# Kernel tuning notes

Measured on AMD Instinct MI355X. Metric: run time of the kernel, lower is better.

Reference implementation:

```python
import jax, jax.numpy as jnp
import numpy as np
from jax import lax

C = 128; G = 8; K = 3; P = K * K; GC = C // G
N, H, W = 4, 96, 96
EPS = 1e-5

def conv_bn_silu(x, w, gamma, beta, rmean, rvar, stride, pad):
    # Conv2d(bias=False) + BatchNorm2d(eval) + SiLU, NCHW
    y = lax.conv_general_dilated(x, w, (stride, stride), [(pad, pad), (pad, pad)],
                                 dimension_numbers=('NCHW', 'OIHW', 'NCHW'))
    s = gamma / jnp.sqrt(rvar + EPS)
    y = y * s[None, :, None, None] + (beta - rmean * s)[None, :, None, None]
    return y * jax.nn.sigmoid(y)

def dcnv3(x, dw_w, dw_b, ln_g, ln_b, off_w, off_b, m_w, m_b, ip_w, ip_b, op_w, op_b):
    # InternImage DCNv3, channels-last input (N,H,W,C), k=3 s=1 pad=1 dil=1 group=G, offset_scale=1
    n, h, w, c = x.shape
    xp = x @ ip_w.T + ip_b  # input_proj
    # offset/mask branch: depthwise 3x3 conv + LayerNorm + GELU on the ORIGINAL input
    dw = lax.conv_general_dilated(x, dw_w, (1, 1), [(1, 1), (1, 1)],
                                  dimension_numbers=('NHWC', 'HWIO', 'NHWC'),
                                  feature_group_count=c) + dw_b
    dw = (dw - dw.mean(-1, keepdims=True)) / jnp.sqrt(dw.var(-1, keepdims=True) + EPS) * ln_g + ln_b
    dw = jax.nn.gelu(dw)
    off = (dw @ off_w.T + off_b).reshape(n, h, w, G, P, 2)  # (..., (dx, dy))
    m = jax.nn.softmax((dw @ m_w.T + m_b).reshape(n, h, w, G, P), -1)
    pad = 1
    hp, wp = h + 2 * pad, w + 2 * pad
    xpad = jnp.pad(xp, ((0, 0), (pad, pad), (pad, pad), (0, 0))).reshape(n, hp, wp, G, GC)
    ky, kx = jnp.meshgrid(jnp.arange(-1, 2, dtype=x.dtype), jnp.arange(-1, 2, dtype=x.dtype), indexing='ij')
    # absolute sampling coords in padded image (grid_sample align_corners=False equivalent)
    py = (jnp.arange(h, dtype=x.dtype) + pad)[None, :, None, None, None] + ky.reshape(-1) + off[..., 1]
    px = (jnp.arange(w, dtype=x.dtype) + pad)[None, None, :, None, None] + kx.reshape(-1) + off[..., 0]
    yf = jnp.floor(py); xf = jnp.floor(px)
    wy = py - yf; wx = px - xf
    y0 = yf.astype(jnp.int32); x0 = xf.astype(jnp.int32)
    n_idx = jnp.arange(n)[:, None, None, None, None]
    g_idx = jnp.arange(G)[None, None, None, :, None]

    def gat(yi, xi):
        valid = ((yi >= 0) & (yi < hp) & (xi >= 0) & (xi < wp)).astype(x.dtype)
        v = xpad[n_idx, jnp.clip(yi, 0, hp - 1), jnp.clip(xi, 0, wp - 1), g_idx]  # (n,h,w,G,P,GC)
        return v * valid[..., None]

    v = (gat(y0, x0) * ((1 - wy) * (1 - wx))[..., None]
         + gat(y0, x0 + 1) * ((1 - wy) * wx)[..., None]
         + gat(y0 + 1, x0) * (wy * (1 - wx))[..., None]
         + gat(y0 + 1, x0 + 1) * (wy * wx)[..., None])
    out = jnp.einsum('nhwgpc,nhwgp->nhwgc', v, m).reshape(n, h, w, c)
    return out @ op_w.T + op_b  # output_proj

def _forward(x0, x1, x2, conv_w, conv_g, conv_b, conv_rm, conv_rv,
             conv1_w, conv1_g, conv1_b, conv1_rm, conv1_rv,
             conv2_w, conv2_g, conv2_b, conv2_rm, conv2_rv,
             dw_w, dw_b, ln_g, ln_b, off_w, off_b, m_w, m_b, ip_w, ip_b, op_w, op_b):
    n, _, h, w = x0.shape
    # x1: 256 ch > 128 -> self.conv (1x1); smaller spatial -> bilinear upsample to HW
    y1 = conv_bn_silu(x1, conv_w, conv_g, conv_b, conv_rm, conv_rv, 1, 0)
    feat_up1 = jax.image.resize(y1, (n, C, h, w), method='bilinear')
    # x2: 64 ch < 128 -> self.conv1 (1x1); larger spatial -> self.conv2 (3x3 s2) to HW
    y2 = conv_bn_silu(x2, conv1_w, conv1_g, conv1_b, conv1_rm, conv1_rv, 1, 0)
    feat_up2 = conv_bn_silu(y2, conv2_w, conv2_g, conv2_b, conv2_rm, conv2_rv, 2, 1)
    d1 = dcnv3(feat_up1.transpose(0, 2, 3, 1), dw_w, dw_b, ln_g, ln_b, off_w, off_b, m_w, m_b, ip_w, ip_b, op_w, op_b)
    d2 = dcnv3(feat_up2.transpose(0, 2, 3, 1), dw_w, dw_b, ln_g, ln_b, off_w, off_b, m_w, m_b, ip_w, ip_b, op_w, op_b)
    a1 = jax.nn.relu(d1).transpose(0, 3, 1, 2)
    a2 = jax.nn.relu(d2).transpose(0, 3, 1, 2)
    return jnp.concatenate([a1, x0, a2], axis=1)  # (N, 3C, H, W)

def setup_inputs():
    ks = jax.random.split(jax.random.key(0), 24)
    f = jnp.float32
    return {
        'x0': jax.random.normal(ks[0], (N, C, H, W), f),
        'x1': jax.random.normal(ks[1], (N, 2 * C, H // 2, W // 2), f),
        'x2': jax.random.normal(ks[2], (N, C // 2, 2 * H, 2 * W), f),
        'conv_w': jax.random.normal(ks[3], (C, 2 * C, 1, 1), f) * 0.05,
        'conv_g': jnp.ones((C,), f), 'conv_b': jnp.zeros((C,), f),
        'conv_rm': jax.random.normal(ks[4], (C,), f) * 0.1,
        'conv_rv': jax.random.uniform(ks[5], (C,), f) + 0.5,
        'conv1_w': jax.random.normal(ks[6], (C, C // 2, 1, 1), f) * 0.08,
        'conv1_g': jnp.ones((C,), f), 'conv1_b': jnp.zeros((C,), f),
        'conv1_rm': jax.random.normal(ks[7], (C,), f) * 0.1,
        'conv1_rv': jax.random.uniform(ks[8], (C,), f) + 0.5,
        'conv2_w': jax.random.normal(ks[9], (C, C, 3, 3), f) * 0.03,
        'conv2_g': jnp.ones((C,), f), 'conv2_b': jnp.zeros((C,), f),
        'conv2_rm': jax.random.normal(ks[10], (C,), f) * 0.1,
        'conv2_rv': jax.random.uniform(ks[11], (C,), f) + 0.5,
        'dw_w': jax.random.normal(ks[12], (3, 3, 1, C), f) * 0.1,
        'dw_b': jnp.zeros((C,), f),
        'ln_g': jnp.ones((C,), f), 'ln_b': jnp.zeros((C,), f),
        'off_w': jax.random.normal(ks[13], (G * P * 2, C), f) * 0.01,
        'off_b': jnp.zeros((G * P * 2,), f),
        'm_w': jax.random.normal(ks[14], (G * P, C), f) * 0.05,
        'm_b': jnp.zeros((G * P,), f),
        'ip_w': jax.random.normal(ks[15], (C, C), f) * 0.05,
        'ip_b': jnp.zeros((C,), f),
        'op_w': jax.random.normal(ks[16], (C, C), f) * 0.05,
        'op_b': jnp.zeros((C,), f),
    }

def reference(x0, x1, x2, conv_w, conv_g, conv_b, conv_rm, conv_rv,
              conv1_w, conv1_g, conv1_b, conv1_rm, conv1_rv,
              conv2_w, conv2_g, conv2_b, conv2_rm, conv2_rv,
              dw_w, dw_b, ln_g, ln_b, off_w, off_b, m_w, m_b, ip_w, ip_b, op_w, op_b):
    return _forward(x0, x1, x2, conv_w, conv_g, conv_b, conv_rm, conv_rv,
                    conv1_w, conv1_g, conv1_b, conv1_rm, conv1_rv,
                    conv2_w, conv2_g, conv2_b, conv2_rm, conv2_rv,
                    dw_w, dw_b, ln_g, ln_b, off_w, off_b, m_w, m_b, ip_w, ip_b, op_w, op_b)
```

## Files before the change

### kernel.cpp

```cpp
#include <hip/hip_runtime.h>
#include <cstdint>
#include <cstddef>

#define EPSV 1e-5f
#define NPIX 9216
#define LDA 136
#define LDK 72

typedef __bf16 bf16;
typedef _Float16 f16;
typedef __attribute__((ext_vector_type(8))) __bf16 bf16x8;
typedef __attribute__((ext_vector_type(4))) __bf16 bf16x4;
typedef __attribute__((ext_vector_type(2))) _Float16 f16x2;
typedef __attribute__((ext_vector_type(4))) float  f32x4;

__device__ __forceinline__ float silu_f(float v) { return v / (1.f + __expf(-v)); }

__global__ __launch_bounds__(256) void prep_kernel(
    const float* __restrict__ conv_w, const float* __restrict__ conv_g,
    const float* __restrict__ conv_b, const float* __restrict__ conv_rm, const float* __restrict__ conv_rv,
    const float* __restrict__ conv1_w, const float* __restrict__ conv1_g,
    const float* __restrict__ conv1_b, const float* __restrict__ conv1_rm, const float* __restrict__ conv1_rv,
    const float* __restrict__ conv2_w, const float* __restrict__ conv2_g,
    const float* __restrict__ conv2_bb, const float* __restrict__ conv2_rm, const float* __restrict__ conv2_rv,
    const float* __restrict__ ip_w, const float* __restrict__ op_w,
    const float* __restrict__ off_w, const float* __restrict__ m_w,
    const float* __restrict__ off_b, const float* __restrict__ m_b,
    float* __restrict__ WTSf, bf16* __restrict__ WTSb)
{
  int idx = blockIdx.x * 256 + threadIdx.x;
  if (idx < 608) {
    if (idx < 128) {
      int co = idx;
      float s = conv_g[co] * rsqrtf(conv_rv[co] + EPSV);
      WTSf[idx] = conv_b[co] - conv_rm[co] * s;
    } else if (idx < 256) {
      int co = idx - 128;
      float s = conv1_g[co] * rsqrtf(conv1_rv[co] + EPSV);
      WTSf[idx] = conv1_b[co] - conv1_rm[co] * s;
    } else if (idx < 384) {
      int co = idx - 256;
      float s = conv2_g[co] * rsqrtf(conv2_rv[co] + EPSV);
      WTSf[idx] = conv2_bb[co] - conv2_rm[co] * s;
    } else {
      int col = idx - 384;
      WTSf[idx] = (col < 144) ? off_b[col] : (col < 216 ? m_b[col - 144] : 0.f);
    }
  } else {
    int j = idx - 608;
    if (j < 32768) {
      int co = j >> 8, ci = j & 255;
      float s = conv_g[co] * rsqrtf(conv_rv[co] + EPSV);
      WTSb[j] = (bf16)(conv_w[co * 256 + ci] * s);
    } else if (j < 40960) {
      int r = j - 32768; int co = r >> 6, ci = r & 63;
      float s = conv1_g[co] * rsqrtf(conv1_rv[co] + EPSV);
      WTSb[j] = (bf16)(conv1_w[co * 64 + ci] * s);
    } else if (j < 188416) {
      int r = j - 40960; int kp = r >> 14; int rr = r & 16383;
      int co = rr >> 7, ci = rr & 127;
      float s = conv2_g[co] * rsqrtf(conv2_rv[co] + EPSV);
      WTSb[j] = (bf16)(conv2_w[(co * 128 + ci) * 9 + kp] * s);
    } else if (j < 204800) {
      int r = j - 188416; int co = r >> 7, ci = r & 127;
      WTSb[j] = (bf16)ip_w[co * 128 + ci];
    } else if (j < 233472) {
      int r = j - 204800; int co = r >> 7, ci = r & 127;
      float v = (co < 144) ? off_w[co * 128 + ci] : (co < 216 ? m_w[(co - 144) * 128 + ci] : 0.f);
      WTSb[j] = (bf16)v;
    } else if (j < 249856) {
      int r = j - 233472; int co = r >> 7, ci = r & 127;
      WTSb[j] = (bf16)op_w[co * 128 + ci];
    }
  }
}

__device__ __forceinline__ void c1x1_body(
    bf16* As, bf16* Bs, const float* __restrict__ x, const bf16* __restrict__ W,
    const float* __restrict__ bias, int K, int HW, int m0, bf16* __restrict__ outb)
{
  int t = threadIdx.x;
  int n = m0 / HW; int hw0 = m0 - n * HW;
  const float* xn = x + (size_t)n * K * HW;
  int wv = t >> 6, lane = t & 63;
  int lrow = lane & 15, q = lane >> 4;
  int n0 = wv * 32;
  f32x4 acc[4][2];
#pragma unroll
  for (int i = 0; i < 4; ++i)
#pragma unroll
    for (int j = 0; j < 2; ++j)
#pragma unroll
      for (int e = 0; e < 4; ++e) acc[i][j][e] = 0.f;

  for (int k0 = 0; k0 < K; k0 += 64) {
    if (k0) __syncthreads();
    for (int i = t; i < 1024; i += 256) {
      int px = i & 63; int ci4 = (i >> 6) << 2;
      bf16x4 p;
#pragma unroll
      for (int j = 0; j < 4; ++j)
        p[j] = (bf16)xn[(size_t)(k0 + ci4 + j) * HW + hw0 + px];
      *(bf16x4*)&As[px * LDK + ci4] = p;
    }
    for (int i = t; i < 1024; i += 256) {
      int co = i >> 3; int k8 = (i & 7) << 3;
      *(bf16x8*)&Bs[co * LDK + k8] = *(const bf16x8*)&W[(size_t)co * K + k0 + k8];
    }
    __syncthreads();
#pragma unroll
    for (int ks = 0; ks < 2; ++ks) {
      int ko = ks * 32 + q * 8;
      bf16x8 bfr0 = *(const bf16x8*)&Bs[(n0 + lrow) * LDK + ko];
      bf16x8 bfr1 = *(const bf16x8*)&Bs[(n0 + 16 + lrow) * LDK + ko];
#pragma unroll
      for (int mi = 0; mi < 4; ++mi) {
        bf16x8 afr = *(const bf16x8*)&As[(mi * 16 + lrow) * LDK + ko];
        acc[mi][0] = __builtin_amdgcn_mfma_f32_16x16x32_bf16(afr, bfr0, acc[mi][0], 0, 0, 0);
        acc[mi][1] = __builtin_amdgcn_mfma_f32_16x16x32_bf16(afr, bfr1, acc[mi][1], 0, 0, 0);
      }
    }
  }
#pragma unroll
  for (int mi = 0; mi < 4; ++mi) {
#pragma unroll
    for (int nj = 0; nj < 2; ++nj) {
      int co = n0 + nj * 16 + lrow;
      float bb = bias[co];
#pragma unroll
      for (int r = 0; r < 4; ++r) {
        int m = m0 + mi * 16 + q * 4 + r;
        outb[(size_t)m * 128 + co] = (bf16)silu_f(acc[mi][nj][r] + bb);
      }
    }
  }
}

__global__ __launch_bounds__(256) void c1x1_dual_kernel(
    const float* __restrict__ x1, const bf16* __restrict__ W1b, const float* __restrict__ b1f,
    const float* __restrict__ x2, const bf16* __restrict__ W1bb, const float* __restrict__ b1bf,
    bf16* __restrict__ y1b, bf16* __restrict__ y2b)
{
  __shared__ bf16 As[64 * LDK];
  __shared__ bf16 Bs[128 * LDK];
  int bid = blockIdx.x;
  if (bid < 2304) {
    c1x1_body(As, Bs, x2, W1bb, b1bf, 64, 36864, bid << 6, y2b);
  } else {
    c1x1_body(As, Bs, x1, W1b, b1f, 256, 2304, (bid - 2304) << 6, y1b);
  }
}

__global__ __launch_bounds__(256) void upsample_kernel(
    const bf16* __restrict__ y1b, bf16* __restrict__ feat1b)
{
  int idx = blockIdx.x * 256 + threadIdx.x;
  int c4 = (idx & 31) << 2;
  int pw = idx >> 5;
  int ow = pw % 96; int t1 = pw / 96;
  int oh = t1 % 96; int n = t1 / 96;
  float sh = oh * 0.5f - 0.25f, sw = ow * 0.5f - 0.25f;
  float hf = floorf(sh), wf = floorf(sw);
  float fy = sh - hf, fx = sw - wf;
  int h0 = (int)hf, w0 = (int)wf;
  int h0c = max(h0, 0), h1c = min(h0 + 1, 47);
  int w0c = max(w0, 0), w1c = min(w0 + 1, 47);
  const bf16* yn = y1b + (size_t)n * 2304 * 128 + c4;
  bf16x4 v00 = *(const bf16x4*)&yn[(h0c * 48 + w0c) * 128];
  bf16x4 v01 = *(const bf16x4*)&yn[(h0c * 48 + w1c) * 128];
  bf16x4 v10 = *(const bf16x4*)&yn[(h1c * 48 + w0c) * 128];
  bf16x4 v11 = *(const bf16x4*)&yn[(h1c * 48 + w1c) * 128];
  bf16x4 o;
#pragma unroll
  for (int e = 0; e < 4; ++e) {
    float v = (1.f - fy) * ((1.f - fx) * (float)v00[e] + fx * (float)v01[e])
            + fy * ((1.f - fx) * (float)v10[e] + fx * (float)v11[e]);
    o[e] = (bf16)v;
  }
  *(bf16x4*)&feat1b[((size_t)n * NPIX + oh * 96 + ow) * 128 + c4] = o;
}

__global__ __launch_bounds__(256) void conv2_mfma_kernel(
    const bf16* __restrict__ y2b, const bf16* __restrict__ W2b,
    const float* __restrict__ b2, bf16* __restrict__ feat2b)
{
  __shared__ bf16 As[64 * LDA];
  __shared__ bf16 Bs[128 * LDA];
  int m0 = blockIdx.x << 6;
  int t = threadIdx.x;
  int wv = t >> 6, lane = t & 63;
  int lrow = lane & 15, q = lane >> 4;
  int n0 = wv * 32;
  f32x4 acc[4][2];
#pragma unroll
  for (int i = 0; i < 4; ++i)
#pragma unroll
    for (int j = 0; j < 2; ++j)
#pragma unroll
      for (int e = 0; e < 4; ++e) acc[i][j][e] = 0.f;
  bf16x8 zv;
#pragma unroll
  for (int e = 0; e < 8; ++e) zv[e] = (bf16)0.f;

  for (int kp = 0; kp < 9; ++kp) {
    int kh = kp / 3, kw = kp - kh * 3;
    __syncthreads();
    for (int i = t; i < 1024; i += 256) {
      int row = i >> 4; int c8 = (i & 15) << 3;
      int m = m0 + row;
      int nimg = m / NPIX; int hw = m - nimg * NPIX;
      int oh = hw / 96, ow = hw - oh * 96;
      int ih = 2 * oh - 1 + kh, iw = 2 * ow - 1 + kw;
      bf16x8 v = zv;
      if ((unsigned)ih < 192u && (unsigned)iw < 192u)
        v = *(const bf16x8*)&y2b[(((size_t)nimg * 192 + ih) * 192 + iw) * 128 + c8];
      *(bf16x8*)&As[row * LDA + c8] = v;
    }
    const bf16* Wk = W2b + kp * 16384;
    for (int i = t; i < 2048; i += 256) {
      int nn = i >> 4; int k8 = (i & 15) << 3;
      *(bf16x8*)&Bs[nn * LDA + k8] = *(const bf16x8*)&Wk[nn * 128 + k8];
    }
    __syncthreads();
#pragma unroll
    for (int ks = 0; ks < 4; ++ks) {
      bf16x8 bfr0 = *(const bf16x8*)&Bs[(n0 + lrow) * LDA + ks * 32 + q * 8];
      bf16x8 bfr1 = *(const bf16x8*)&Bs[(n0 + 16 + lrow) * LDA + ks * 32 + q * 8];
#pragma unroll
      for (int mi = 0; mi < 4; ++mi) {
        bf16x8 afr = *(const bf16x8*)&As[(mi * 16 + lrow) * LDA + ks * 32 + q * 8];
        acc[mi][0] = __builtin_amdgcn_mfma_f32_16x16x32_bf16(afr, bfr0, acc[mi][0], 0, 0, 0);
        acc[mi][1] = __builtin_amdgcn_mfma_f32_16x16x32_bf16(afr, bfr1, acc[mi][1], 0, 0, 0);
      }
    }
  }
#pragma unroll
  for (int mi = 0; mi < 4; ++mi) {
#pragma unroll
    for (int nj = 0; nj < 2; ++nj) {
      int co = n0 + nj * 16 + lrow;
      float bb = b2[co];
#pragma unroll
      for (int r = 0; r < 4; ++r) {
        int m = m0 + mi * 16 + q * 4 + r;
        feat2b[(size_t)m * 128 + co] = (bf16)silu_f(acc[mi][nj][r] + bb);
      }
    }
  }
}

__global__ __launch_bounds__(256) void mm_ip_kernel(
    const bf16* __restrict__ A, const bf16* __restrict__ W,
    const float* __restrict__ bias, bf16* __restrict__ outb)
{
  __shared__ bf16 As[64 * LDA];
  __shared__ bf16 Bs[128 * LDA];
  int m0 = blockIdx.x << 6;
  int t = threadIdx.x;
  for (int i = t; i < 1024; i += 256) {
    int row = i >> 4; int c8 = (i & 15) << 3;
    *(bf16x8*)&As[row * LDA + c8] = *(const bf16x8*)&A[(size_t)(m0 + row) * 128 + c8];
  }
  for (int i = t; i < 2048; i += 256) {
    int n = i >> 4; int k8 = (i & 15) << 3;
    *(bf16x8*)&Bs[n * LDA + k8] = *(const bf16x8*)&W[(size_t)n * 128 + k8];
  }
  __syncthreads();

  int wv = t >> 6, lane = t & 63;
  int lrow = lane & 15, q = lane >> 4;
  int n0 = wv * 32;
  f32x4 acc[4][2];
#pragma unroll
  for (int i = 0; i < 4; ++i)
#pragma unroll
    for (int j = 0; j < 2; ++j)
#pragma unroll
      for (int e = 0; e < 4; ++e) acc[i][j][e] = 0.f;

#pragma unroll
  for (int ks = 0; ks < 4; ++ks) {
    bf16x8 bfr0 = *(const bf16x8*)&Bs[(n0 + lrow) * LDA + ks * 32 + q * 8];
    bf16x8 bfr1 = *(const bf16x8*)&Bs[(n0 + 16 + lrow) * LDA + ks * 32 + q * 8];
#pragma unroll
    for (int mi = 0; mi < 4; ++mi) {
      bf16x8 afr = *(const bf16x8*)&As[(mi * 16 + lrow) * LDA + ks * 32 + q * 8];
      acc[mi][0] = __builtin_amdgcn_mfma_f32_16x16x32_bf16(afr, bfr0, acc[mi][0], 0, 0, 0);
      acc[mi][1] = __builtin_amdgcn_mfma_f32_16x16x32_bf16(afr, bfr1, acc[mi][1], 0, 0, 0);
    }
  }
#pragma unroll
  for (int mi = 0; mi < 4; ++mi) {
#pragma unroll
    for (int nj = 0; nj < 2; ++nj) {
      int col = n0 + nj * 16 + lrow;
      float bb = bias[col];
#pragma unroll
      for (int r = 0; r < 4; ++r) {
        int m = m0 + mi * 16 + q * 4 + r;
        outb[(size_t)m * 128 + col] = (bf16)(acc[mi][nj][r] + bb);
      }
    }
  }
}

__global__ __launch_bounds__(256) void dwom_kernel(
    const bf16* __restrict__ featb, const float* __restrict__ dw_w,
    const float* __restrict__ dw_b, const float* __restrict__ ln_g,
    const float* __restrict__ ln_b, const bf16* __restrict__ Wom,
    const float* __restrict__ bom, f16* __restrict__ offm)
{
  __shared__ float Wts[1152];
  __shared__ float Pb[384];
  __shared__ bf16 Ds[16 * LDA];
  int t = threadIdx.x;
  for (int i = t; i < 1152; i += 256) Wts[i] = dw_w[i];
  for (int i = t; i < 384; i += 256)
    Pb[i] = (i < 128) ? dw_b[i] : (i < 256 ? ln_g[i - 128] : ln_b[i - 256]);
  __syncthreads();

  int bid = blockIdx.x;
  int wg = (bid & 7) * 576 + (bid >> 3);
  {
    int pxl = t >> 4;
    int c8 = (t & 15) << 3;
    int pixel = wg * 16 + pxl;
    int n = pixel / NPIX; int hw = pixel - n * NPIX;
    int h = hw / 96; int w = hw - h * 96;
    const bf16* fn = featb + (size_t)n * NPIX * 128 + c8;
    bf16x8 zv;
#pragma unroll
    for (int e = 0; e < 8; ++e) zv[e] = (bf16)0.f;

    bf16x8 v[9];
#pragma unroll
    for (int p = 0; p < 9; ++p) {
      int hh = h + p / 3 - 1, ww = w + (p % 3) - 1;
      bool valid = ((unsigned)hh < 96u) && ((unsigned)ww < 96u);
      int hc = min(max(hh, 0), 95), wc = min(max(ww, 0), 95);
      bf16x8 x = *(const bf16x8*)&fn[(hc * 96 + wc) * 128];
      v[p] = valid ? x : zv;
    }

    float acc[8];
#pragma unroll
    for (int e = 0; e < 8; ++e) acc[e] = Pb[c8 + e];
#pragma unroll
    for (int p = 0; p < 9; ++p) {
      f32x4 w0 = *(const f32x4*)&Wts[p * 128 + c8];
      f32x4 w1 = *(const f32x4*)&Wts[p * 128 + c8 + 4];
#pragma unroll
      for (int e = 0; e < 4; ++e) {
        acc[e]     += (float)v[p][e]     * w0[e];
        acc[4 + e] += (float)v[p][4 + e] * w1[e];
      }
    }

    float s = 0.f, qs = 0.f;
#pragma unroll
    for (int e = 0; e < 8; ++e) { s += acc[e]; qs += acc[e] * acc[e]; }
#pragma unroll
    for (int off = 8; off > 0; off >>= 1) {
      s  += __shfl_xor(s, off);
      qs += __shfl_xor(qs, off);
    }
    float mean = s * (1.f / 128.f);
    float var = qs * (1.f / 128.f) - mean * mean;
    float rstd = rsqrtf(var + EPSV);
    bf16x8 o;
#pragma unroll
    for (int e = 0; e < 8; ++e) {
      float xn = (acc[e] - mean) * rstd * Pb[128 + c8 + e] + Pb[256 + c8 + e];
      float z = 0.7978845608028654f * (xn + 0.044715f * xn * xn * xn);
      float th;
      if (z > 15.f) th = 1.f;
      else if (z < -15.f) th = -1.f;
      else { float e2 = __expf(2.f * z); th = (e2 - 1.f) / (e2 + 1.f); }
      o[e] = (bf16)(0.5f * xn * (1.f + th));
    }
    *(bf16x8*)&Ds[pxl * LDA + c8] = o;
  }
  __syncthreads();

  {
    int wv = t >> 6, lane = t & 63;
    int lrow = lane & 15, q = lane >> 4;
    f16* orow = offm + (size_t)(wg * 16) * 224;
    for (int gsel = wv; gsel < 7; gsel += 4) {
      int n0 = gsel * 32;
      f32x4 pacc[2];
#pragma unroll
      for (int j = 0; j < 2; ++j)
#pragma unroll
        for (int e = 0; e < 4; ++e) pacc[j][e] = 0.f;
#pragma unroll
      for (int ks = 0; ks < 4; ++ks) {
        int ko = ks * 32 + q * 8;
        bf16x8 afr  = *(const bf16x8*)&Ds[lrow * LDA + ko];
        bf16x8 bfr0 = *(const bf16x8*)&Wom[(size_t)(n0 + lrow) * 128 + ko];
        bf16x8 bfr1 = *(const bf16x8*)&Wom[(size_t)(n0 + 16 + lrow) * 128 + ko];
        pacc[0] = __builtin_amdgcn_mfma_f32_16x16x32_bf16(afr, bfr0, pacc[0], 0, 0, 0);
        pacc[1] = __builtin_amdgcn_mfma_f32_16x16x32_bf16(afr, bfr1, pacc[1], 0, 0, 0);
      }
#pragma unroll
      for (int nj = 0; nj < 2; ++nj) {
        int col = n0 + nj * 16 + lrow;
        float bb = bom[col];
#pragma unroll
        for (int r = 0; r < 4; ++r) {
          int px = q * 4 + r;
          orow[(size_t)px * 224 + col] = (f16)(pacc[nj][r] + bb);
        }
      }
    }
  }
}

__global__ __launch_bounds__(512, 6) void sample_copy_kernel(
    const bf16* __restrict__ xpb, const f16* __restrict__ offm,
    const bf16* __restrict__ Wop, const float* __restrict__ op_b,
    const float4* __restrict__ x0, float* __restrict__ out)
{
  __shared__ char LB[32256];
  int t = threadIdx.x;
  int bid = blockIdx.x;
  if (bid >= 2304) {
    int idx = (bid - 2304) * 512 + t;
    int n = idx / (128 * 2304);
    int r = idx - n * (128 * 2304);
    float4* outv = (float4*)out;
    outv[(size_t)(n * 384 + 128) * 2304 + r] = x0[(size_t)n * 128 * 2304 + r];
    return;
  }
  uint32_t* Sd = (uint32_t*)LB;
  float*    Pm = (float*)(LB + 14336);
  bf16*     Avs = (bf16*)(LB + 23552);
  float*    Cs = (float*)LB;
  const f16* S = (const f16*)Sd;
  int wg = (bid & 7) * 288 + (bid >> 3);
  {
    const uint32_t* src = (const uint32_t*)(offm + (size_t)wg * 32 * 224);
    for (int i = t; i < 3584; i += 512) Sd[i] = src[i];
  }
  __syncthreads();
  if (t < 256) {
    int px = t >> 3, gg = t & 7;
    const f16* L = S + px * 224 + 144 + gg * 9;
    float l[9]; float mx = -1e30f;
#pragma unroll
    for (int p = 0; p < 9; ++p) { l[p] = (float)L[p]; mx = fmaxf(mx, l[p]); }
    float se = 0.f;
#pragma unroll
    for (int p = 0; p < 9; ++p) { l[p] = __expf(l[p] - mx); se += l[p]; }
    float inv = 1.f / se;
    float* Pp = Pm + px * 72 + gg * 9;
#pragma unroll
    for (int p = 0; p < 9; ++p) Pp[p] = l[p] * inv;
  }
  __syncthreads();
  {
    int pxl = t >> 4;
    int tid16 = t & 15;
    int g = tid16 >> 1;
    int c8 = (tid16 & 1) << 3;
    int pixel = wg * 32 + pxl;
    int n = pixel / NPIX; int hw = pixel - n * NPIX;
    int h = hw / 96; int w = hw - h * 96;
    const f16* Sp = S + pxl * 224 + g * 18;
    const float* Pp = Pm + pxl * 72 + g * 9;
    const bf16* xpn = xpb + (size_t)n * NPIX * 128 + g * 16 + c8;
    float acc[8];
#pragma unroll
    for (int e = 0; e < 8; ++e) acc[e] = 0.f;
#pragma unroll 1
    for (int kh = 0; kh < 3; ++kh) {
#pragma unroll
      for (int kw = 0; kw < 3; ++kw) {
        int p = kh * 3 + kw;
        f16x2 d2 = *(const f16x2*)&Sp[p * 2];
        float dx = (float)d2.x, dy = (float)d2.y;
        float pyu = (float)(h + kh - 1) + dy;
        float pxu = (float)(w + kw - 1) + dx;
        float yf = floorf(pyu), xf = floorf(pxu);
        float wy = pyu - yf, wx = pxu - xf;
        int y0 = (int)yf, x0i = (int)xf;
        float ay0 = ((unsigned)y0 < 96u) ? (1.f - wy) : 0.f;
        float ay1 = ((unsigned)(y0 + 1) < 96u) ? wy : 0.f;
        float ax0 = ((unsigned)x0i < 96u) ? (1.f - wx) : 0.f;
        float ax1 = ((unsigned)(x0i + 1) < 96u) ? wx : 0.f;
        int y0c = min(max(y0, 0), 95), y1c = min(max(y0 + 1, 0), 95);
        int x0c = min(max(x0i, 0), 95), x1c = min(max(x0i + 1, 0), 95);
        float mp = Pp[p];
        float w00 = ay0 * ax0 * mp, w01 = ay0 * ax1 * mp;
        float w10 = ay1 * ax0 * mp, w11 = ay1 * ax1 * mp;
        bf16x8 v00 = *(const bf16x8*)&xpn[(y0c * 96 + x0c) * 128];
        bf16x8 v01 = *(const bf16x8*)&xpn[(y0c * 96 + x1c) * 128];
        bf16x8 v10 = *(const bf16x8*)&xpn[(y1c * 96 + x0c) * 128];
        bf16x8 v11 = *(const bf16x8*)&xpn[(y1c * 96 + x1c) * 128];
#pragma unroll
        for (int e = 0; e < 8; ++e) {
          acc[e] += w00 * (float)v00[e] + w01 * (float)v01[e]
                  + w10 * (float)v10[e] + w11 * (float)v11[e];
        }
      }
    }
    bf16x8 o;
#pragma unroll
    for (int e = 0; e < 8; ++e) o[e] = (bf16)acc[e];
    *(bf16x8*)&Avs[pxl * LDA + g * 16 + c8] = o;
  }
  __syncthreads();

  {
    int wv = t >> 6, lane = t & 63;
    int lrow = lane & 15, q = lane >> 4;
    int mrow0 = (wv & 1) * 16;
    int n0 = (wv >> 1) * 32;
    f32x4 pacc[2];
#pragma unroll
    for (int j = 0; j < 2; ++j)
#pragma unroll
      for (int e = 0; e < 4; ++e) pacc[j][e] = 0.f;
#pragma unroll
    for (int ks = 0; ks < 4; ++ks) {
      int ko = ks * 32 + q * 8;
      bf16x8 afr  = *(const bf16x8*)&Avs[(mrow0 + lrow) * LDA + ko];
      bf16x8 bfr0 = *(const bf16x8*)&Wop[(size_t)(n0 + lrow) * 128 + ko];
      bf16x8 bfr1 = *(const bf16x8*)&Wop[(size_t)(n0 + 16 + lrow) * 128 + ko];
      pacc[0] = __builtin_amdgcn_mfma_f32_16x16x32_bf16(afr, bfr0, pacc[0], 0, 0, 0);
      pacc[1] = __builtin_amdgcn_mfma_f32_16x16x32_bf16(afr, bfr1, pacc[1], 0, 0, 0);
    }
#pragma unroll
    for (int nj = 0; nj < 2; ++nj) {
      int col = n0 + nj * 16 + lrow;
      float bb = op_b[col];
#pragma unroll
      for (int r = 0; r < 4; ++r) {
        int px = mrow0 + q * 4 + r;
        Cs[col * 33 + px] = fmaxf(pacc[nj][r] + bb, 0.f);
      }
    }
  }
  __syncthreads();

  {
    int nn = (wg * 32) / NPIX;
    int hwb = wg * 32 - nn * NPIX;
    int img = nn & 3; int choff = (nn >= 4) ? 256 : 0;
    float* ob = out + (size_t)(img * 384 + choff) * NPIX + hwb;
#pragma unroll
    for (int i = t; i < 1024; i += 512) {
      int col = i >> 3, f4 = i & 7;
      f32x4 v = *(const f32x4*)&Cs[col * 33 + f4 * 4];
      *(f32x4*)&ob[(size_t)col * NPIX + f4 * 4] = v;
    }
  }
}

extern "C" void kernel_launch(void* const* d_in, const int* in_sizes, int n_in,
                              void* d_out, int out_size, void* d_ws, size_t ws_size,
                              hipStream_t stream)
{
  (void)in_sizes; (void)n_in; (void)out_size; (void)ws_size;
  const float* x0      = (const float*)d_in[0];
  const float* x1      = (const float*)d_in[1];
  const float* x2      = (const float*)d_in[2];
  const float* conv_w  = (const float*)d_in[3];
  const float* conv_g  = (const float*)d_in[4];
  const float* conv_b  = (const float*)d_in[5];
  const float* conv_rm = (const float*)d_in[6];
  const float* conv_rv = (const float*)d_in[7];
  const float* conv1_w = (const float*)d_in[8];
  const float* conv1_g = (const float*)d_in[9];
  const float* conv1_b = (const float*)d_in[10];
  const float* conv1_rm= (const float*)d_in[11];
  const float* conv1_rv= (const float*)d_in[12];
  const float* conv2_w = (const float*)d_in[13];
  const float* conv2_g = (const float*)d_in[14];
  const float* conv2_b = (const float*)d_in[15];
  const float* conv2_rm= (const float*)d_in[16];
  const float* conv2_rv= (const float*)d_in[17];
  const float* dw_w    = (const float*)d_in[18];
  const float* dw_b    = (const float*)d_in[19];
  const float* ln_g    = (const float*)d_in[20];
  const float* ln_b    = (const float*)d_in[21];
  const float* off_w   = (const float*)d_in[22];
  const float* off_b   = (const float*)d_in[23];
  const float* m_w     = (const float*)d_in[24];
  const float* m_b     = (const float*)d_in[25];
  const float* ip_w    = (const float*)d_in[26];
  const float* ip_b    = (const float*)d_in[27];
  const float* op_w    = (const float*)d_in[28];
  const float* op_b    = (const float*)d_in[29];
  float* out = (float*)d_out;
  char* WS = (char*)d_ws;

  bf16* featb  = (bf16*)WS;
  bf16* feat1b = featb;
  bf16* feat2b = featb + 4718592;
  bf16* y2b    = (bf16*)(WS + 18874368);
  bf16* xpb    = (bf16*)(WS + 18874368);
  bf16* y1b    = (bf16*)(WS + 56623104);
  f16*  offm   = (f16*)(WS + 58982400);
  float* WTSf  = (float*)(WS + 125042688);
  bf16*  WTSb  = (bf16*)(WS + 125045120);

  float* b1f  = WTSf;
  float* b1bf = WTSf + 128;
  float* b2f  = WTSf + 256;
  float* bomf = WTSf + 384;
  bf16* W1b  = WTSb;
  bf16* W1bb = WTSb + 32768;
  bf16* W2b  = WTSb + 40960;
  bf16* Wipb = WTSb + 188416;
  bf16* Womb = WTSb + 204800;
  bf16* Wopb = WTSb + 233472;

  prep_kernel<<<979, 256, 0, stream>>>(
      conv_w, conv_g, conv_b, conv_rm, conv_rv,
      conv1_w, conv1_g, conv1_b, conv1_rm, conv1_rv,
      conv2_w, conv2_g, conv2_b, conv2_rm, conv2_rv,
      ip_w, op_w, off_w, m_w, off_b, m_b, WTSf, WTSb);

  c1x1_dual_kernel<<<2448, 256, 0, stream>>>(x1, W1b, b1f, x2, W1bb, b1bf, y1b, y2b);

  upsample_kernel<<<4608, 256, 0, stream>>>(y1b, feat1b);
  conv2_mfma_kernel<<<576, 256, 0, stream>>>(y2b, W2b, b2f, feat2b);

  mm_ip_kernel<<<1152, 256, 0, stream>>>(featb, Wipb, ip_b, xpb);
  dwom_kernel<<<4608, 256, 0, stream>>>(featb, dw_w, dw_b, ln_g, ln_b, Womb, bomf, offm);

  sample_copy_kernel<<<4608, 512, 0, stream>>>(xpb, offm, Wopb, op_b,
                                               (const float4*)x0, out);
}
```

Measured before the change: 355.5 us.

## Merge input-projection GEMM into depthwise offset/mask kernel as extra blocks

Removes the separate mm_ip_kernel launch and appends 4608 extra blocks to the dwom kernel that each compute a 16-pixel input_proj GEMM tile, reading weight fragments straight from global memory instead of staging them in LDS. The intent is to drop one launch and let both independent workloads share the GPU concurrently within one grid. The cost is that weights are reused far less per block (16 rows instead of 64), so global/L2 weight traffic rises, and LDS is shared through a union buffer.

```diff
diff --git a/kernel.cpp b/kernel.cpp
--- a/kernel.cpp
+++ b/kernel.cpp
@@ -249,77 +249,74 @@
   }
 }
 
-__global__ __launch_bounds__(256) void mm_ip_kernel(
-    const bf16* __restrict__ A, const bf16* __restrict__ W,
-    const float* __restrict__ bias, bf16* __restrict__ outb)
-{
-  __shared__ bf16 As[64 * LDA];
-  __shared__ bf16 Bs[128 * LDA];
-  int m0 = blockIdx.x << 6;
-  int t = threadIdx.x;
-  for (int i = t; i < 1024; i += 256) {
-    int row = i >> 4; int c8 = (i & 15) << 3;
-    *(bf16x8*)&As[row * LDA + c8] = *(const bf16x8*)&A[(size_t)(m0 + row) * 128 + c8];
-  }
-  for (int i = t; i < 2048; i += 256) {
-    int n = i >> 4; int k8 = (i & 15) << 3;
-    *(bf16x8*)&Bs[n * LDA + k8] = *(const bf16x8*)&W[(size_t)n * 128 + k8];
-  }
-  __syncthreads();
-
-  int wv = t >> 6, lane = t & 63;
-  int lrow = lane & 15, q = lane >> 4;
-  int n0 = wv * 32;
-  f32x4 acc[4][2];
-#pragma unroll
-  for (int i = 0; i < 4; ++i)
-#pragma unroll
-    for (int j = 0; j < 2; ++j)
-#pragma unroll
-      for (int e = 0; e < 4; ++e) acc[i][j][e] = 0.f;
-
-#pragma unroll
-  for (int ks = 0; ks < 4; ++ks) {
-    bf16x8 bfr0 = *(const bf16x8*)&Bs[(n0 + lrow) * LDA + ks * 32 + q * 8];
-    bf16x8 bfr1 = *(const bf16x8*)&Bs[(n0 + 16 + lrow) * LDA + ks * 32 + q * 8];
-#pragma unroll
-    for (int mi = 0; mi < 4; ++mi) {
-      bf16x8 afr = *(const bf16x8*)&As[(mi * 16 + lrow) * LDA + ks * 32 + q * 8];
-      acc[mi][0] = __builtin_amdgcn_mfma_f32_16x16x32_bf16(afr, bfr0, acc[mi][0], 0, 0, 0);
-      acc[mi][1] = __builtin_amdgcn_mfma_f32_16x16x32_bf16(afr, bfr1, acc[mi][1], 0, 0, 0);
-    }
-  }
-#pragma unroll
-  for (int mi = 0; mi < 4; ++mi) {
-#pragma unroll
-    for (int nj = 0; nj < 2; ++nj) {
-      int col = n0 + nj * 16 + lrow;
-      float bb = bias[col];
-#pragma unroll
-      for (int r = 0; r < 4; ++r) {
-        int m = m0 + mi * 16 + q * 4 + r;
-        outb[(size_t)m * 128 + col] = (bf16)(acc[mi][nj][r] + bb);
-      }
-    }
-  }
-}
-
-__global__ __launch_bounds__(256) void dwom_kernel(
+__global__ __launch_bounds__(256) void dwom_ip_kernel(
     const bf16* __restrict__ featb, const float* __restrict__ dw_w,
     const float* __restrict__ dw_b, const float* __restrict__ ln_g,
     const float* __restrict__ ln_b, const bf16* __restrict__ Wom,
-    const float* __restrict__ bom, f16* __restrict__ offm)
-{
-  __shared__ float Wts[1152];
-  __shared__ float Pb[384];
-  __shared__ bf16 Ds[16 * LDA];
+    const float* __restrict__ bom, const bf16* __restrict__ Wip,
+    const float* __restrict__ ip_b, f16* __restrict__ offm,
+    bf16* __restrict__ xpb)
+{
+  __shared__ char LB[10496];
   int t = threadIdx.x;
+  int bid = blockIdx.x;
+
+  if (bid >= 4608) {
+    bf16* Ds = (bf16*)LB;
+    bf16* Xs = (bf16*)(LB + 4352);
+    int pixel0 = (bid - 4608) * 16;
+    {
+      int pxl = t >> 4;
+      int c8 = (t & 15) << 3;
+      *(bf16x8*)&Ds[pxl * LDA + c8] =
+          *(const bf16x8*)&featb[(size_t)(pixel0 + pxl) * 128 + c8];
+    }
+    __syncthreads();
+    {
+      int wv = t >> 6, lane = t & 63;
+      int lrow = lane & 15, q = lane >> 4;
+      int n0 = wv * 32;
+      f32x4 pacc[2];
+#pragma unroll
+      for (int j = 0; j < 2; ++j)
+#pragma unroll
+        for (int e = 0; e < 4; ++e) pacc[j][e] = 0.f;
+#pragma unroll
+      for (int ks = 0; ks < 4; ++ks) {
+        int ko = ks * 32 + q * 8;
+        bf16x8 afr  = *(const bf16x8*)&Ds[lrow * LDA + ko];
+        bf16x8 bfr0 = *(const bf16x8*)&Wip[(size_t)(n0 + lrow) * 128 + ko];
+        bf16x8 bfr1 = *(const bf16x8*)&Wip[(size_t)(n0 + 16 + lrow) * 128 + ko];
+        pacc[0] = __builtin_amdgcn_mfma_f32_16x16x32_bf16(afr, bfr0, pacc[0], 0, 0, 0);
+        pacc[1] = __builtin_amdgcn_mfma_f32_16x16x32_bf16(afr, bfr1, pacc[1], 0, 0, 0);
+      }
+#pragma unroll
+      for (int nj = 0; nj < 2; ++nj) {
+        int col = n0 + nj * 16 + lrow;
+        float bb = ip_b[col];
+#pragma unroll
+        for (int r = 0; r < 4; ++r)
+          Xs[(q * 4 + r) * LDA + col] = (bf16)(pacc[nj][r] + bb);
+      }
+    }
+    __syncthreads();
+    {
+      int pxl = t >> 4;
+      int c8 = (t & 15) << 3;
+      *(bf16x8*)&xpb[(size_t)(pixel0 + pxl) * 128 + c8] =
+          *(const bf16x8*)&Xs[pxl * LDA + c8];
+    }
+    return;
+  }
+
+  float* Wts = (float*)LB;
+  float* Pb  = (float*)(LB + 4608);
+  bf16*  Ds  = (bf16*)(LB + 6144);
   for (int i = t; i < 1152; i += 256) Wts[i] = dw_w[i];
   for (int i = t; i < 384; i += 256)
     Pb[i] = (i < 128) ? dw_b[i] : (i < 256 ? ln_g[i - 128] : ln_b[i - 256]);
   __syncthreads();
 
-  int bid = blockIdx.x;
   int wg = (bid & 7) * 576 + (bid >> 3);
   {
     int pxl = t >> 4;
@@ -627,8 +624,8 @@
   upsample_kernel<<<4608, 256, 0, stream>>>(y1b, feat1b);
   conv2_mfma_kernel<<<576, 256, 0, stream>>>(y2b, W2b, b2f, feat2b);
 
-  mm_ip_kernel<<<1152, 256, 0, stream>>>(featb, Wipb, ip_b, xpb);
-  dwom_kernel<<<4608, 256, 0, stream>>>(featb, dw_w, dw_b, ln_g, ln_b, Womb, bomf, offm);
+  dwom_ip_kernel<<<9216, 256, 0, stream>>>(featb, dw_w, dw_b, ln_g, ln_b,
+                                           Womb, bomf, Wipb, ip_b, offm, xpb);
 
   sample_copy_kernel<<<4608, 512, 0, stream>>>(xpb, offm, Wopb, op_b,
                                                (const float4*)x0, out);
```

New measurement: 356.7 us (median of 2 runs). Within noise of the previous version (+0.3%).
